# Kernel tuning notes

Hardware: AMD Instinct MI355X
Metric: run time of the kernel (lower is better)

## Reference

```python
import jax, jax.numpy as jnp
import numpy as np

# Longformer-style attention: blocked sliding-window (radius W) + attention to
# the first G global tokens. Source class body was truncated, so this follows
# the canonical Longformer local+global formulation.
B, S, D = 2, 4096, 1024
H, DH = 16, 64          # num_heads, head_dim (H*DH == D)
W = 256                  # one-sided window radius == block size
G = 64                   # number of global tokens (prefix)


def setup_inputs() -> dict:
    key = jax.random.key(0)
    ks = jax.random.split(key, 5)
    x = jax.random.normal(ks[0], (B, S, D), jnp.float32)
    init = 0.02
    Wq = jax.random.normal(ks[1], (D, D), jnp.float32) * init
    Wk = jax.random.normal(ks[2], (D, D), jnp.float32) * init
    Wv = jax.random.normal(ks[3], (D, D), jnp.float32) * init
    Wo = jax.random.normal(ks[4], (D, D), jnp.float32) * init
    return {"x": x, "Wq": Wq, "Wk": Wk, "Wv": Wv, "Wo": Wo}


def _split_heads(t):
    # [B,S,D] -> [B,H,S,DH]
    return t.reshape(B, S, H, DH).transpose(0, 2, 1, 3)


def _local_mask():
    nb = S // W
    blk = jnp.arange(nb)[:, None, None]
    qi = jnp.arange(W)[None, :, None]
    kj = jnp.arange(3 * W)[None, None, :]
    i_abs = blk * W + qi                    # absolute query index
    j_abs = blk * W - W + kj                # absolute key index in 3-block strip
    return ((j_abs >= 0) & (j_abs < S) &
            (jnp.abs(j_abs - i_abs) <= W) &
            (j_abs >= G))                    # global keys handled separately


def reference(x, Wq, Wk, Wv, Wo):
    nb = S // W
    scale = 1.0 / np.sqrt(DH).astype(np.float32)
    q = _split_heads(x @ Wq)                 # [B,H,S,DH]
    k = _split_heads(x @ Wk)
    v = _split_heads(x @ Wv)

    qb = q.reshape(B, H, nb, W, DH)
    pad = ((0, 0), (0, 0), (1, 1), (0, 0), (0, 0))
    kp = jnp.pad(k.reshape(B, H, nb, W, DH), pad)
    vp = jnp.pad(v.reshape(B, H, nb, W, DH), pad)
    # 3-block strips: [B,H,nb,3W,DH]
    k3 = jnp.concatenate([kp[:, :, :-2], kp[:, :, 1:-1], kp[:, :, 2:]], axis=3)
    v3 = jnp.concatenate([vp[:, :, :-2], vp[:, :, 1:-1], vp[:, :, 2:]], axis=3)

    s_loc = jnp.einsum('bhnqd,bhnkd->bhnqk', qb, k3) * scale  # [B,H,nb,W,3W]
    s_loc = jnp.where(_local_mask()[None, None], s_loc, jnp.float32(-1e9))

    kg, vg = k[:, :, :G], v[:, :, :G]        # global prefix tokens
    s_glb = jnp.einsum('bhnqd,bhgd->bhnqg', qb, kg) * scale    # [B,H,nb,W,G]

    p = jax.nn.softmax(jnp.concatenate([s_loc, s_glb], axis=-1), axis=-1)
    p_loc, p_glb = p[..., :3 * W], p[..., 3 * W:]

    out = (jnp.einsum('bhnqk,bhnkd->bhnqd', p_loc, v3) +
           jnp.einsum('bhnqg,bhgd->bhnqd', p_glb, vg))         # [B,H,nb,W,DH]
    out = out.reshape(B, H, S, DH).transpose(0, 2, 1, 3).reshape(B, S, D)
    return out @ Wo
```

## Files before the change

kernel.cpp:

```cpp
#include <hip/hip_runtime.h>

#define BB   2
#define SS   4096
#define DD   1024
#define HH   16
#define DHH  64
#define WW   256
#define GG   64
#define NBLK 16

typedef unsigned short ushort_t;
typedef short  s16x8 __attribute__((ext_vector_type(8)));
typedef float  f32x4 __attribute__((ext_vector_type(4)));

#define QSCALE 0.18033688011112042f

__device__ __forceinline__ ushort_t f2b(float f) {
  unsigned int u = __builtin_bit_cast(unsigned int, f);
  unsigned int r = (u + 0x7fffu + ((u >> 16) & 1u)) >> 16;
  return (ushort_t)r;
}

__device__ __forceinline__ ushort_t f2b1(float f) {
  unsigned int r;
  asm("v_cvt_pk_bf16_f32 %0, %1, %2" : "=v"(r) : "v"(f), "v"(f));
  return (ushort_t)r;
}

__device__ __forceinline__ float exp2f_fast(float x) {
  return __builtin_amdgcn_exp2f(x);
}

__device__ __forceinline__ void gld16(const void* g, void* l) {
  __builtin_amdgcn_global_load_lds(
      (const __attribute__((address_space(1))) void*)g,
      (__attribute__((address_space(3))) void*)l, 16, 0, 0);
}

__global__ __launch_bounds__(256) void xcast(
    const float* __restrict__ x, ushort_t* __restrict__ xb) {
  size_t i = ((size_t)blockIdx.x * 256 + threadIdx.x) * 8;
  float4 f0 = *(const float4*)&x[i];
  float4 f1 = *(const float4*)&x[i + 4];
  ushort_t t[8];
  t[0] = f2b(f0.x); t[1] = f2b(f0.y); t[2] = f2b(f0.z); t[3] = f2b(f0.w);
  t[4] = f2b(f1.x); t[5] = f2b(f1.y); t[6] = f2b(f1.z); t[7] = f2b(f1.w);
  *(uint4*)&xb[i] = *(const uint4*)t;
}

__global__ __launch_bounds__(256) void transpose_w(
    const float* __restrict__ Wq, const float* __restrict__ Wk,
    const float* __restrict__ Wv, const float* __restrict__ Wo,
    ushort_t* __restrict__ outBase) {
  const float* src = (blockIdx.z == 0) ? Wq : (blockIdx.z == 1) ? Wk
                    : (blockIdx.z == 2) ? Wv : Wo;
  ushort_t* dst = outBase + (size_t)blockIdx.z * (1024 * 1024);
  __shared__ __align__(16) ushort_t t[64][72];
  const int tid = threadIdx.x;
  const int bx = blockIdx.x * 64, by = blockIdx.y * 64;
  const int c4 = (tid & 15) * 4;
  const int r16 = tid >> 4;
  for (int rr = r16; rr < 64; rr += 16) {
    float4 f = *(const float4*)&src[(size_t)(by + rr) * 1024 + bx + c4];
    t[c4 + 0][rr] = f2b(f.x);
    t[c4 + 1][rr] = f2b(f.y);
    t[c4 + 2][rr] = f2b(f.z);
    t[c4 + 3][rr] = f2b(f.w);
  }
  __syncthreads();
  const int sr = tid >> 3;
  const int sc = (tid & 7) * 8;
  for (int rr = sr; rr < 64; rr += 32) {
    *(uint4*)&dst[(size_t)(bx + rr) * 1024 + by + sc] = *(const uint4*)&t[rr][sc];
  }
}

template <int MODE>
__global__ __launch_bounds__(512, 2) void gemm256(
    const ushort_t* __restrict__ A, const ushort_t* __restrict__ Bt,
    ushort_t* __restrict__ O0, ushort_t* __restrict__ O1,
    ushort_t* __restrict__ O2, float* __restrict__ Of, int K) {
  __shared__ __align__(16) ushort_t As[2][2][256 * 32];
  __shared__ __align__(16) ushort_t Bs[2][2][256 * 32];

  const int tid  = threadIdx.x;
  const int lane = tid & 63;
  const int w    = tid >> 6;
  const int quad = lane >> 4;
  const int l16  = lane & 15;
  const int wr   = w >> 2;
  const int wc   = w & 3;
  const int bm   = blockIdx.x * 256;
  const int bn   = blockIdx.y * 256;

  const int srow = tid >> 2;
  const int sch  = (tid & 3) ^ ((srow >> 1) & 3);
  const ushort_t* Ag = A + (size_t)(bm + srow) * K + sch * 8;
  const ushort_t* Bg = Bt + (size_t)(bn + srow) * K + sch * 8;

  const int chofs = ((quad ^ ((l16 >> 1) & 3)) << 3);

  auto stage = [&](ushort_t* slab, const ushort_t* g) {
    gld16(g, &slab[tid * 8]);
    gld16(g + (size_t)128 * K, &slab[4096 + tid * 8]);
  };

  f32x4 acc[8][4] = {};
  s16x8 afrag[4], bfrag[4];

  auto ldA = [&](int buf, int kkh, int i) {
    const int row = wr * 128 + i * 16 + l16;
    return *(const s16x8*)&As[buf][kkh][row * 32 + chofs];
  };
  auto ldB = [&](int buf, int kkh, int j) {
    const int row = wc * 64 + j * 16 + l16;
    return *(const s16x8*)&Bs[buf][kkh][row * 32 + chofs];
  };
  auto mfma16 = [&](int ih) {
    __builtin_amdgcn_s_setprio(1);
#pragma unroll
    for (int t = 0; t < 4; t++)
#pragma unroll
      for (int j = 0; j < 4; j++)
        acc[ih * 4 + t][j] = __builtin_amdgcn_mfma_f32_16x16x32_bf16(
            afrag[t], bfrag[j], acc[ih * 4 + t][j], 0, 0, 0);
    __builtin_amdgcn_s_setprio(0);
  };

  const int NT = K >> 6;

  stage(&Bs[0][0][0], Bg);
  stage(&As[0][0][0], Ag);
  stage(&Bs[0][1][0], Bg + 32);
  stage(&As[0][1][0], Ag + 32);
  asm volatile("s_waitcnt vmcnt(4)" ::: "memory");
  stage(&Bs[1][0][0], Bg + 64);
  stage(&As[1][0][0], Ag + 64);
  stage(&Bs[1][1][0], Bg + 96);
  asm volatile("s_waitcnt vmcnt(6)" ::: "memory");
  __builtin_amdgcn_s_barrier();

#pragma unroll 1
  for (int kt = 0; kt < NT; ++kt) {
    const int buf = kt & 1;
#pragma unroll
    for (int j = 0; j < 4; j++) bfrag[j] = ldB(buf, 0, j);
#pragma unroll
    for (int t = 0; t < 4; t++) afrag[t] = ldA(buf, 0, t);
    if (kt + 1 < NT) stage(&As[buf ^ 1][1][0], Ag + (size_t)(kt + 1) * 64 + 32);
    __builtin_amdgcn_s_barrier();
    asm volatile("s_waitcnt lgkmcnt(0)" ::: "memory");
    mfma16(0);
    __builtin_amdgcn_s_barrier();
#pragma unroll
    for (int t = 0; t < 4; t++) afrag[t] = ldA(buf, 0, 4 + t);
    if (kt + 2 < NT) stage(&Bs[buf][0][0], Bg + (size_t)(kt + 2) * 64);
    __builtin_amdgcn_s_barrier();
    asm volatile("s_waitcnt lgkmcnt(0)" ::: "memory");
    mfma16(1);
    __builtin_amdgcn_s_barrier();
#pragma unroll
    for (int j = 0; j < 4; j++) bfrag[j] = ldB(buf, 1, j);
#pragma unroll
    for (int t = 0; t < 4; t++) afrag[t] = ldA(buf, 1, t);
    if (kt + 2 < NT) stage(&As[buf][0][0], Ag + (size_t)(kt + 2) * 64);
    __builtin_amdgcn_s_barrier();
    asm volatile("s_waitcnt lgkmcnt(0)" ::: "memory");
    mfma16(0);
    __builtin_amdgcn_s_barrier();
#pragma unroll
    for (int t = 0; t < 4; t++) afrag[t] = ldA(buf, 1, 4 + t);
    if (kt + 2 < NT) {
      stage(&Bs[buf][1][0], Bg + (size_t)(kt + 2) * 64 + 32);
      asm volatile("s_waitcnt vmcnt(6)" ::: "memory");
    } else if (kt + 1 < NT) {
      asm volatile("s_waitcnt vmcnt(0)" ::: "memory");
    }
    __builtin_amdgcn_s_barrier();
    asm volatile("s_waitcnt lgkmcnt(0)" ::: "memory");
    mfma16(1);
    __builtin_amdgcn_s_barrier();
  }

#pragma unroll
  for (int i = 0; i < 8; i++) {
#pragma unroll
    for (int j = 0; j < 4; j++) {
#pragma unroll
      for (int r = 0; r < 4; r++) {
        int m = bm + wr * 128 + i * 16 + quad * 4 + r;
        int n = bn + wc * 64 + j * 16 + l16;
        float av = acc[i][j][r];
        if (MODE == 0) {
          int n1 = n & 1023;
          int h = n1 >> 6, dh = n1 & 63;
          int b = m >> 12, s = m & 4095;
          if (n < 1024) {
            O0[(((size_t)b * HH + h) * SS + s) * DHH + dh] = f2b(av * QSCALE);
          } else if (n < 2048) {
            O1[(((size_t)b * HH + h) * SS + s) * DHH + dh] = f2b(av);
          } else {
            O2[(((size_t)b * HH + h) * DHH + dh) * SS + s] = f2b(av);
          }
        } else {
          Of[(size_t)m * DD + n] = av;
        }
      }
    }
  }
}

__global__ __launch_bounds__(256, 2) void attn_kernel(
    const ushort_t* __restrict__ q, const ushort_t* __restrict__ k,
    const ushort_t* __restrict__ vT, ushort_t* __restrict__ out) {
  const int blk = blockIdx.x;
  const int h   = blockIdx.y;
  const int b   = blockIdx.z;
  const int tid  = threadIdx.x;
  const int lane = tid & 63;
  const int w    = tid >> 6;
  const int quad = lane >> 4;
  const int l16  = lane & 15;

  const size_t bh = ((size_t)b * HH + h) * SS * DHH;
  const ushort_t* qb  = q + bh;
  const ushort_t* kb  = k + bh;
  const ushort_t* vtb = vT + bh;

  __shared__ __align__(16) ushort_t Ps[4][64 * 64];
  ushort_t* Pw = &Ps[w][0];

  const int q0 = blk * WW + w * 64;

  const int wbase = ((l16 >> 3) << 9) + (quad << 5) + (l16 & 7);
  const int rbase = (quad << 9) + (l16 << 3);

  s16x8 aq[4][2];
#pragma unroll
  for (int mt = 0; mt < 4; mt++)
#pragma unroll
    for (int x = 0; x < 2; x++)
      aq[mt][x] = *(const s16x8*)&qb[(size_t)(q0 + mt * 16 + l16) * DHH + x * 32 + quad * 8];

  f32x4 oacc[4][4] = {};
  f32x4 rsacc[4] = {};

  s16x8 vone;
#pragma unroll
  for (int j = 0; j < 8; j++) vone[j] = (short)0x3F80;

  s16x8 bk[4][2];
  s16x8 bv[4][2];

  auto LOADK = [&](int j0s) {
    const ushort_t* kc = kb + (size_t)j0s * DHH;
#pragma unroll
    for (int nt = 0; nt < 4; nt++)
#pragma unroll
      for (int x = 0; x < 2; x++)
        bk[nt][x] = *(const s16x8*)&kc[(nt * 16 + l16) * DHH + x * 32 + quad * 8];
  };
  auto LOADV = [&](int j0s) {
    const ushort_t* vc = vtb + j0s;
#pragma unroll
    for (int dt = 0; dt < 4; dt++)
#pragma unroll
      for (int x = 0; x < 2; x++)
        bv[dt][x] = *(const s16x8*)&vc[(size_t)(dt * 16 + l16) * SS + x * 32 + quad * 8];
  };

  const int jlo = (q0 - (int)WW < (int)GG) ? (int)GG : (q0 - (int)WW);
  int jhi = q0 + (int)WW;
  if (jhi > SS - 64) jhi = SS - 64;

  int j0  = jlo;
  int j0u = __builtin_amdgcn_readfirstlane(j0);
  LOADK(j0u);

  bool last = false;
  while (!last) {
    int jn = j0 + 64;
    if (j0 == 0) { last = true; jn = 0; }
    else if (jn > jhi) jn = 0;

    LOADV(j0u);

    const int dlt = j0 - q0;
    const bool needmask = (j0 != 0) && (dlt < -193 || dlt > 193);

#pragma unroll
    for (int nt = 0; nt < 4; nt++) {
      const int j = j0 + nt * 16 + l16;
#pragma unroll
      for (int mt = 0; mt < 4; mt++) {
        f32x4 s4 = {0.f, 0.f, 0.f, 0.f};
        s4 = __builtin_amdgcn_mfma_f32_16x16x32_bf16(aq[mt][0], bk[nt][0], s4, 0, 0, 0);
        s4 = __builtin_amdgcn_mfma_f32_16x16x32_bf16(aq[mt][1], bk[nt][1], s4, 0, 0, 0);
#pragma unroll
        for (int r = 0; r < 4; r++) {
          float p;
          if (needmask) {
            int i = q0 + mt * 16 + quad * 4 + r;
            int d = j - i;
            p = (d <= (int)WW && d >= -(int)WW) ? exp2f_fast(s4[r]) : 0.0f;
          } else {
            p = exp2f_fast(s4[r]);
          }
          Pw[wbase + nt * 1024 + mt * 128 + r * 8] = f2b1(p);
        }
      }
    }

    int jnu = __builtin_amdgcn_readfirstlane(jn);
    if (!last) LOADK(jnu);

    __builtin_amdgcn_s_setprio(1);
#pragma unroll
    for (int ll = 0; ll < 64; ll += 32) {
      s16x8 ap[4];
#pragma unroll
      for (int mt = 0; mt < 4; mt++)
        ap[mt] = *(const s16x8*)&Pw[rbase + (ll >> 3) * 512 + mt * 128];
#pragma unroll
      for (int mt = 0; mt < 4; mt++) {
        rsacc[mt] = __builtin_amdgcn_mfma_f32_16x16x32_bf16(ap[mt], vone, rsacc[mt], 0, 0, 0);
#pragma unroll
        for (int dt = 0; dt < 4; dt++)
          oacc[mt][dt] = __builtin_amdgcn_mfma_f32_16x16x32_bf16(ap[mt], bv[dt][ll >> 5], oacc[mt][dt], 0, 0, 0);
      }
    }
    __builtin_amdgcn_s_setprio(0);

    j0 = jn; j0u = jnu;
  }

#pragma unroll
  for (int mt = 0; mt < 4; mt++) {
#pragma unroll
    for (int r = 0; r < 4; r++) {
      float inv = __builtin_amdgcn_rcpf(rsacc[mt][r]);
      int srow2 = q0 + mt * 16 + quad * 4 + r;
      size_t orow = ((size_t)b * SS + srow2) * DD + h * DHH;
#pragma unroll
      for (int dt = 0; dt < 4; dt++)
        out[orow + dt * 16 + l16] = f2b1(oacc[mt][dt][r] * inv);
    }
  }
}

extern "C" void kernel_launch(void* const* d_in, const int* in_sizes, int n_in,
                              void* d_out, int out_size, void* d_ws, size_t ws_size,
                              hipStream_t stream) {
  const float *x, *Wq, *Wk, *Wv, *Wo;
  if (n_in == 5 && in_sizes[4] == 8388608) {
    Wk = (const float*)d_in[0]; Wo = (const float*)d_in[1];
    Wq = (const float*)d_in[2]; Wv = (const float*)d_in[3];
    x  = (const float*)d_in[4];
  } else {
    x  = (const float*)d_in[0]; Wq = (const float*)d_in[1];
    Wk = (const float*)d_in[2]; Wv = (const float*)d_in[3];
    Wo = (const float*)d_in[4];
  }
  float* out = (float*)d_out;

  char* ws = (char*)d_ws;
  ushort_t* wqkvT = (ushort_t*)(ws);
  ushort_t* woT   = (ushort_t*)(ws + 6291456);
  ushort_t* qbuf  = (ushort_t*)(ws + 8388608);
  ushort_t* kbuf  = (ushort_t*)(ws + 8388608 + 16777216);
  ushort_t* vbuf  = (ushort_t*)(ws + 8388608 + 2 * 16777216);
  ushort_t* attn  = (ushort_t*)(ws + 8388608 + 3 * 16777216);
  ushort_t* xb    = attn;

  xcast<<<dim3(4096), 256, 0, stream>>>(x, xb);
  transpose_w<<<dim3(16, 16, 4), 256, 0, stream>>>(Wq, Wk, Wv, Wo, wqkvT);
  gemm256<0><<<dim3(32, 12), 512, 0, stream>>>(xb, wqkvT, qbuf, kbuf, vbuf, nullptr, 1024);
  attn_kernel<<<dim3(NBLK, HH, BB), 256, 0, stream>>>(qbuf, kbuf, vbuf, attn);
  gemm256<1><<<dim3(32, 4), 512, 0, stream>>>(attn, woT, nullptr, nullptr, nullptr, out, 1024);
}
```

Before: 272.7 us.

## Stage transposed V epilogue through LDS and remap blocks per XCD

The GEMM epilogue for the V-transposed output now writes accumulators into shared memory, transposes there, and stores 16-byte vectors along the sequence dimension. The old path issued scattered 2-byte stores with a stride of the sequence length. Shared memory is merged into one flat buffer so the epilogue can reuse it. Block indices are also remapped so consecutive M tiles land on the same XCD, which is meant to improve L2 reuse. The trade-offs are extra barriers in the epilogue and the assumption that the grid size divides evenly by 8 and 4.

```diff
diff --git a/kernel.cpp b/kernel.cpp
--- a/kernel.cpp
+++ b/kernel.cpp
@@ -80,8 +80,7 @@
     const ushort_t* __restrict__ A, const ushort_t* __restrict__ Bt,
     ushort_t* __restrict__ O0, ushort_t* __restrict__ O1,
     ushort_t* __restrict__ O2, float* __restrict__ Of, int K) {
-  __shared__ __align__(16) ushort_t As[2][2][256 * 32];
-  __shared__ __align__(16) ushort_t Bs[2][2][256 * 32];
+  __shared__ __align__(16) ushort_t SH[65536];
 
   const int tid  = threadIdx.x;
   const int lane = tid & 63;
@@ -90,8 +89,21 @@
   const int l16  = lane & 15;
   const int wr   = w >> 2;
   const int wc   = w & 3;
-  const int bm   = blockIdx.x * 256;
-  const int bn   = blockIdx.y * 256;
+
+  const int id  = blockIdx.x + (gridDim.x * blockIdx.y);
+  const int xcd = id & 7;
+  const int seq = id >> 3;
+  const int nx  = (xcd << 2) + (seq & 3);
+  const int ny  = seq >> 2;
+  const int bm  = nx * 256;
+  const int bn  = ny * 256;
+
+  auto Aslab = [&](int buf, int kkh) -> ushort_t* {
+    return &SH[(buf * 2 + kkh) * 8192];
+  };
+  auto Bslab = [&](int buf, int kkh) -> ushort_t* {
+    return &SH[32768 + (buf * 2 + kkh) * 8192];
+  };
 
   const int srow = tid >> 2;
   const int sch  = (tid & 3) ^ ((srow >> 1) & 3);
@@ -110,11 +122,11 @@
 
   auto ldA = [&](int buf, int kkh, int i) {
     const int row = wr * 128 + i * 16 + l16;
-    return *(const s16x8*)&As[buf][kkh][row * 32 + chofs];
+    return *(const s16x8*)&Aslab(buf, kkh)[row * 32 + chofs];
   };
   auto ldB = [&](int buf, int kkh, int j) {
     const int row = wc * 64 + j * 16 + l16;
-    return *(const s16x8*)&Bs[buf][kkh][row * 32 + chofs];
+    return *(const s16x8*)&Bslab(buf, kkh)[row * 32 + chofs];
   };
   auto mfma16 = [&](int ih) {
     __builtin_amdgcn_s_setprio(1);
@@ -129,14 +141,14 @@
 
   const int NT = K >> 6;
 
-  stage(&Bs[0][0][0], Bg);
-  stage(&As[0][0][0], Ag);
-  stage(&Bs[0][1][0], Bg + 32);
-  stage(&As[0][1][0], Ag + 32);
+  stage(Bslab(0, 0), Bg);
+  stage(Aslab(0, 0), Ag);
+  stage(Bslab(0, 1), Bg + 32);
+  stage(Aslab(0, 1), Ag + 32);
   asm volatile("s_waitcnt vmcnt(4)" ::: "memory");
-  stage(&Bs[1][0][0], Bg + 64);
-  stage(&As[1][0][0], Ag + 64);
-  stage(&Bs[1][1][0], Bg + 96);
+  stage(Bslab(1, 0), Bg + 64);
+  stage(Aslab(1, 0), Ag + 64);
+  stage(Bslab(1, 1), Bg + 96);
   asm volatile("s_waitcnt vmcnt(6)" ::: "memory");
   __builtin_amdgcn_s_barrier();
 
@@ -147,14 +159,14 @@
     for (int j = 0; j < 4; j++) bfrag[j] = ldB(buf, 0, j);
 #pragma unroll
     for (int t = 0; t < 4; t++) afrag[t] = ldA(buf, 0, t);
-    if (kt + 1 < NT) stage(&As[buf ^ 1][1][0], Ag + (size_t)(kt + 1) * 64 + 32);
+    if (kt + 1 < NT) stage(Aslab(buf ^ 1, 1), Ag + (size_t)(kt + 1) * 64 + 32);
     __builtin_amdgcn_s_barrier();
     asm volatile("s_waitcnt lgkmcnt(0)" ::: "memory");
     mfma16(0);
     __builtin_amdgcn_s_barrier();
 #pragma unroll
     for (int t = 0; t < 4; t++) afrag[t] = ldA(buf, 0, 4 + t);
-    if (kt + 2 < NT) stage(&Bs[buf][0][0], Bg + (size_t)(kt + 2) * 64);
+    if (kt + 2 < NT) stage(Bslab(buf, 0), Bg + (size_t)(kt + 2) * 64);
     __builtin_amdgcn_s_barrier();
     asm volatile("s_waitcnt lgkmcnt(0)" ::: "memory");
     mfma16(1);
@@ -163,7 +175,7 @@
     for (int j = 0; j < 4; j++) bfrag[j] = ldB(buf, 1, j);
 #pragma unroll
     for (int t = 0; t < 4; t++) afrag[t] = ldA(buf, 1, t);
-    if (kt + 2 < NT) stage(&As[buf][0][0], Ag + (size_t)(kt + 2) * 64);
+    if (kt + 2 < NT) stage(Aslab(buf, 0), Ag + (size_t)(kt + 2) * 64);
     __builtin_amdgcn_s_barrier();
     asm volatile("s_waitcnt lgkmcnt(0)" ::: "memory");
     mfma16(0);
@@ -171,7 +183,7 @@
 #pragma unroll
     for (int t = 0; t < 4; t++) afrag[t] = ldA(buf, 1, 4 + t);
     if (kt + 2 < NT) {
-      stage(&Bs[buf][1][0], Bg + (size_t)(kt + 2) * 64 + 32);
+      stage(Bslab(buf, 1), Bg + (size_t)(kt + 2) * 64 + 32);
       asm volatile("s_waitcnt vmcnt(6)" ::: "memory");
     } else if (kt + 1 < NT) {
       asm volatile("s_waitcnt vmcnt(0)" ::: "memory");
@@ -182,28 +194,56 @@
     __builtin_amdgcn_s_barrier();
   }
 
-#pragma unroll
-  for (int i = 0; i < 8; i++) {
-#pragma unroll
-    for (int j = 0; j < 4; j++) {
-#pragma unroll
-      for (int r = 0; r < 4; r++) {
-        int m = bm + wr * 128 + i * 16 + quad * 4 + r;
-        int n = bn + wc * 64 + j * 16 + l16;
-        float av = acc[i][j][r];
-        if (MODE == 0) {
-          int n1 = n & 1023;
-          int h = n1 >> 6, dh = n1 & 63;
-          int b = m >> 12, s = m & 4095;
-          if (n < 1024) {
-            O0[(((size_t)b * HH + h) * SS + s) * DHH + dh] = f2b(av * QSCALE);
-          } else if (n < 2048) {
-            O1[(((size_t)b * HH + h) * SS + s) * DHH + dh] = f2b(av);
+  if (MODE == 0 && bn >= 2048) {
+    const int bb = bm >> 12;
+    const int n1b = bn & 1023;
+    const int sb  = bm & 4095;
+#pragma unroll 1
+    for (int p = 0; p < 2; p++) {
+      __syncthreads();
+      if (wr == p) {
+#pragma unroll
+        for (int i = 0; i < 8; i++)
+#pragma unroll
+          for (int j = 0; j < 4; j++)
+#pragma unroll
+            for (int r = 0; r < 4; r++)
+              SH[(wc * 64 + j * 16 + l16) * 136 + i * 16 + quad * 4 + r] =
+                  f2b(acc[i][j][r]);
+      }
+      __syncthreads();
+#pragma unroll
+      for (int it = 0; it < 8; it++) {
+        const int row = it * 32 + (tid >> 4);
+        const int n1 = n1b + row;
+        const int dh = n1 & 63, hh = n1 >> 6;
+        const int s = sb + p * 128 + (tid & 15) * 8;
+        uint4 val = *(const uint4*)&SH[row * 136 + (tid & 15) * 8];
+        *(uint4*)&O2[(((size_t)bb * HH + hh) * DHH + dh) * SS + s] = val;
+      }
+    }
+  } else {
+#pragma unroll
+    for (int i = 0; i < 8; i++) {
+#pragma unroll
+      for (int j = 0; j < 4; j++) {
+#pragma unroll
+        for (int r = 0; r < 4; r++) {
+          int m = bm + wr * 128 + i * 16 + quad * 4 + r;
+          int n = bn + wc * 64 + j * 16 + l16;
+          float av = acc[i][j][r];
+          if (MODE == 0) {
+            int n1 = n & 1023;
+            int h = n1 >> 6, dh = n1 & 63;
+            int b = m >> 12, s = m & 4095;
+            if (n < 1024) {
+              O0[(((size_t)b * HH + h) * SS + s) * DHH + dh] = f2b(av * QSCALE);
+            } else {
+              O1[(((size_t)b * HH + h) * SS + s) * DHH + dh] = f2b(av);
+            }
           } else {
-            O2[(((size_t)b * HH + h) * DHH + dh) * SS + s] = f2b(av);
+            Of[(size_t)m * DD + n] = av;
           }
-        } else {
-          Of[(size_t)m * DD + n] = av;
         }
       }
     }
```

Result: faster. 245.9 us (-9.8%).
